# Performance work log

Measured on AMD Instinct MI355X. Metric: run time of the kernel, lower is better.

## Reference

```python
import jax, jax.numpy as jnp
import numpy as np

BATCH, HID, STEPS = 64, 2048, 30

def setup_inputs() -> dict:
    key = jax.random.key(0)
    ks = jax.random.split(key, 7)
    s = 1.0 / np.sqrt(HID)  # pytorch LSTM/Linear init scale
    return {
        "monthly_token": jax.random.normal(ks[0], (BATCH, HID), jnp.float32),
        "steps": STEPS,
        "W_ih": jax.random.uniform(ks[1], (4 * HID, HID), jnp.float32, -s, s),
        "W_hh": jax.random.uniform(ks[2], (4 * HID, HID), jnp.float32, -s, s),
        "b_ih": jax.random.uniform(ks[3], (4 * HID,), jnp.float32, -s, s),
        "b_hh": jax.random.uniform(ks[4], (4 * HID,), jnp.float32, -s, s),
        "W_out": jax.random.uniform(ks[5], (1, HID), jnp.float32, -s, s),
        "b_out": jax.random.uniform(ks[6], (1,), jnp.float32, -s, s),
    }

def reference(monthly_token, steps, W_ih, W_hh, b_ih, b_hh, W_out, b_out):
    H = monthly_token.shape[1]
    h0 = monthly_token                      # (B, H) initial hidden
    c0 = jnp.zeros_like(h0)
    x0 = jnp.zeros_like(h0)                 # first lstm input is zeros

    def step(carry, _):
        h, c, x = carry
        # PyTorch gate order: input, forget, cell(g), output
        gates = x @ W_ih.T + b_ih + h @ W_hh.T + b_hh   # (B, 4H)
        i, f, g, o = jnp.split(gates, 4, axis=-1)
        i = jax.nn.sigmoid(i)
        f = jax.nn.sigmoid(f)
        g = jnp.tanh(g)
        o = jax.nn.sigmoid(o)
        c_new = f * c + i * g
        h_new = o * jnp.tanh(c_new)
        y = h_new @ W_out.T + b_out          # (B, 1) daily value
        # feedback: next input is the lstm output (= h_new for 1-layer LSTM)
        return (h_new, c_new, h_new), y[:, 0]

    _, ys = jax.lax.scan(step, (h0, c0, x0), xs=None, length=steps)
    return ys.T                               # (B, steps)
```

## Files before the change

kernel.cpp:

```cpp
#include <hip/hip_runtime.h>
#include <cmath>


#define HID   2048
#define BATCH 64
#define G4    8192
#define NCU   256
#define HGRP  (HID * BATCH / 8)

typedef __attribute__((ext_vector_type(8))) _Float16 half8;
typedef __attribute__((ext_vector_type(4))) float f32x4;

#define LDS_BYTES 160768

__global__ void k_init(const float* __restrict__ token, const float* __restrict__ bih,
                       const float* __restrict__ bhh, half8* __restrict__ h0p,
                       float* __restrict__ bsum, unsigned* __restrict__ flags) {
    int g = blockIdx.x * 256 + threadIdx.x;
    int l = g & 63, nt = (g >> 6) & 3, kt = g >> 8;
    int n = nt * 16 + (l & 15);
    int k0 = kt * 32 + (l >> 4) * 8;
    const float4* ps = (const float4*)(token + (size_t)n * HID + k0);
    float4 a = ps[0], b = ps[1];
    half8 v;
    v[0]=(_Float16)a.x; v[1]=(_Float16)a.y; v[2]=(_Float16)a.z; v[3]=(_Float16)a.w;
    v[4]=(_Float16)b.x; v[5]=(_Float16)b.y; v[6]=(_Float16)b.z; v[7]=(_Float16)b.w;
    h0p[g] = v;
    if (g < G4) bsum[g] = bih[g] + bhh[g];
    if (g < NCU) flags[g] = 0u;
}

__global__ __launch_bounds__(512, 2)
void k_lstm(const float* __restrict__ wih, const float* __restrict__ whh,
            const float* __restrict__ bsum, const float* __restrict__ wout,
            _Float16* __restrict__ hbuf,
            float* __restrict__ ypart,
            unsigned* __restrict__ flags, int steps) {
    extern __shared__ char smem[];
    half8*     Wlds   = (half8*)smem;
    float*     gates  = (float*)(smem + 131072);
    f32x4*     red4   = (f32x4*)(smem + 139264);
    float*     cbuf   = (float*)(smem + 155648);
    float*     ybuf   = (float*)(smem + 157696);
    _Float16*  hstage = (_Float16*)(smem + 159744);

    const int tid  = threadIdx.x;
    const int blk  = blockIdx.x;
    const int lane = tid & 63;
    const int w    = tid >> 6;
    const int half = w & 1;
    const int ks   = w >> 1;

    for (int idx = tid; idx < 2 * 64 * 64; idx += 512) {
        int l = idx & 63, kt = (idx >> 6) & 63, m2 = idx >> 12;
        int m = l & 15;
        int gate = m2 * 2 + (m >> 3);
        int row  = gate * HID + blk * 8 + (m & 7);
        int col  = kt * 32 + (l >> 4) * 8;
        const float4* p = (const float4*)(whh + (size_t)row * HID + col);
        float4 a = p[0], b = p[1];
        half8 v;
        v[0]=(_Float16)a.x; v[1]=(_Float16)a.y; v[2]=(_Float16)a.z; v[3]=(_Float16)a.w;
        v[4]=(_Float16)b.x; v[5]=(_Float16)b.y; v[6]=(_Float16)b.z; v[7]=(_Float16)b.w;
        Wlds[idx] = v;
    }
    cbuf[tid] = 0.0f;

    float bias_r[2][4];
    if (ks == 0) {
        const int q = lane >> 4;
        #pragma unroll
        for (int mt2 = 0; mt2 < 2; ++mt2)
            #pragma unroll
            for (int r = 0; r < 4; ++r) {
                int m16 = q * 4 + r;
                bias_r[mt2][r] = bsum[(mt2 * 2 + (m16 >> 3)) * HID + blk * 8 + (m16 & 7)];
            }
    }
    const float wj = wout[blk * 8 + w];
    __syncthreads();

    for (int t = 0; t < steps; ++t) {
        const half8* hp = (const half8*)(hbuf + (size_t)t * HID * BATCH);
        f32x4 a00 = {0,0,0,0}, a01 = {0,0,0,0}, a10 = {0,0,0,0}, a11 = {0,0,0,0};
        const int ktb = ks * 16;
        #pragma unroll 8
        for (int kk = 0; kk < 16; ++kk) {
            int kt = ktb + kk;
            half8 av0 = Wlds[(kt) * 64 + lane];
            half8 av1 = Wlds[(64 + kt) * 64 + lane];
            half8 b0  = hp[(kt * 4 + half * 2 + 0) * 64 + lane];
            half8 b1  = hp[(kt * 4 + half * 2 + 1) * 64 + lane];
            a00 = __builtin_amdgcn_mfma_f32_16x16x32_f16(av0, b0, a00, 0, 0, 0);
            a01 = __builtin_amdgcn_mfma_f32_16x16x32_f16(av0, b1, a01, 0, 0, 0);
            a10 = __builtin_amdgcn_mfma_f32_16x16x32_f16(av1, b0, a10, 0, 0, 0);
            a11 = __builtin_amdgcn_mfma_f32_16x16x32_f16(av1, b1, a11, 0, 0, 0);
        }
        if (ks == 1 || ks == 3) {
            int srow = (ks == 3 ? 2 : 0) + half;
            red4[(srow * 4 + 0) * 64 + lane] = a00;
            red4[(srow * 4 + 1) * 64 + lane] = a01;
            red4[(srow * 4 + 2) * 64 + lane] = a10;
            red4[(srow * 4 + 3) * 64 + lane] = a11;
        }
        __syncthreads();
        if (ks == 0 || ks == 2) {
            int srow = (ks == 2 ? 2 : 0) + half;
            a00 += red4[(srow * 4 + 0) * 64 + lane];
            a01 += red4[(srow * 4 + 1) * 64 + lane];
            a10 += red4[(srow * 4 + 2) * 64 + lane];
            a11 += red4[(srow * 4 + 3) * 64 + lane];
        }
        __syncthreads();
        if (ks == 2) {
            red4[(half * 4 + 0) * 64 + lane] = a00;
            red4[(half * 4 + 1) * 64 + lane] = a01;
            red4[(half * 4 + 2) * 64 + lane] = a10;
            red4[(half * 4 + 3) * 64 + lane] = a11;
        }
        __syncthreads();
        if (ks == 0) {
            a00 += red4[(half * 4 + 0) * 64 + lane];
            a01 += red4[(half * 4 + 1) * 64 + lane];
            a10 += red4[(half * 4 + 2) * 64 + lane];
            a11 += red4[(half * 4 + 3) * 64 + lane];
            const int q = lane >> 4, col = lane & 15;
            #pragma unroll
            for (int r = 0; r < 4; ++r) {
                float* g0 = gates + (q * 4 + r) * 64 + (half * 2) * 16 + col;
                float* g1 = gates + (16 + q * 4 + r) * 64 + (half * 2) * 16 + col;
                g0[0]  = a00[r] + bias_r[0][r];
                g0[16] = a01[r] + bias_r[0][r];
                g1[0]  = a10[r] + bias_r[1][r];
                g1[16] = a11[r] + bias_r[1][r];
            }
        }
        __syncthreads();
        {
            const int b = lane;
            float gi = gates[(0  + w) * 64 + b];
            float gf = gates[(8  + w) * 64 + b];
            float gg = gates[(16 + w) * 64 + b];
            float go = gates[(24 + w) * 64 + b];
            float iv = 1.0f / (1.0f + __expf(-gi));
            float fv = 1.0f / (1.0f + __expf(-gf));
            float gv = tanhf(gg);
            float ov = 1.0f / (1.0f + __expf(-go));
            float cn = fv * cbuf[w * 64 + b] + iv * gv;
            cbuf[w * 64 + b] = cn;
            float hv = ov * tanhf(cn);
            hstage[b * 8 + w] = (_Float16)hv;
            ybuf[w * 64 + b]  = hv * wj;
        }
        __syncthreads();
        if (tid < 64) {
            float s = ybuf[tid];
            #pragma unroll
            for (int u = 1; u < 8; ++u) s += ybuf[u * 64 + tid];
            ypart[((size_t)t * NCU + blk) * 64 + tid] = s;
            const int b = tid;
            const int kt = blk >> 2, quad = blk & 3;
            const int nt = b >> 4, lp = quad * 16 + (b & 15);
            const size_t g = (size_t)(kt * 4 + nt) * 64 + lp;
            unsigned long long* dst = (unsigned long long*)
                (hbuf + (size_t)(t + 1) * HID * BATCH + g * 8);
            const unsigned long long* src =
                (const unsigned long long*)(hstage + b * 8);
            unsigned long long v0 = src[0], v1 = src[1];
            __hip_atomic_store(dst,     v0, __ATOMIC_RELAXED, __HIP_MEMORY_SCOPE_AGENT);
            __hip_atomic_store(dst + 1, v1, __ATOMIC_RELAXED, __HIP_MEMORY_SCOPE_AGENT);
        }
        if (t == 0) {
            for (int idx = tid; idx < 2 * 64 * 64; idx += 512) {
                int l = idx & 63, kt = (idx >> 6) & 63, m2 = idx >> 12;
                int m = l & 15;
                int gate = m2 * 2 + (m >> 3);
                int row  = gate * HID + blk * 8 + (m & 7);
                int col  = kt * 32 + (l >> 4) * 8;
                const float4* p = (const float4*)(wih + (size_t)row * HID + col);
                float4 a = p[0], b = p[1];
                half8 v = Wlds[idx];
                v[0] = (_Float16)((float)v[0] + a.x); v[1] = (_Float16)((float)v[1] + a.y);
                v[2] = (_Float16)((float)v[2] + a.z); v[3] = (_Float16)((float)v[3] + a.w);
                v[4] = (_Float16)((float)v[4] + b.x); v[5] = (_Float16)((float)v[5] + b.y);
                v[6] = (_Float16)((float)v[6] + b.z); v[7] = (_Float16)((float)v[7] + b.w);
                Wlds[idx] = v;
            }
        }
        if (t < steps - 1) {
            if (tid < 64) asm volatile("s_waitcnt vmcnt(0)" ::: "memory");
            if (tid == 0)
                __hip_atomic_store(&flags[blk], (unsigned)(t + 1),
                                   __ATOMIC_RELAXED, __HIP_MEMORY_SCOPE_AGENT);
            if (tid < NCU) {
                while (__hip_atomic_load(&flags[tid], __ATOMIC_RELAXED,
                                         __HIP_MEMORY_SCOPE_AGENT) <= (unsigned)t)
                    __builtin_amdgcn_s_sleep(1);
            }
            __syncthreads();
        }
    }
}

__global__ void k_yout(const float* __restrict__ ypart, const float* __restrict__ bout,
                       float* __restrict__ out, int steps) {
    int t = blockIdx.x;
    int b = threadIdx.x;
    const float* p = ypart + (size_t)t * NCU * 64 + b;
    float s = bout[0];
    #pragma unroll 8
    for (int cu = 0; cu < NCU; ++cu) s += p[(size_t)cu * 64];
    out[(size_t)b * steps + t] = s;
}

extern "C" void kernel_launch(void* const* d_in, const int* in_sizes, int n_in,
                              void* d_out, int out_size, void* d_ws, size_t ws_size,
                              hipStream_t stream) {
    const float* token = (const float*)d_in[0];
    const float* wih   = (const float*)d_in[2];
    const float* whh   = (const float*)d_in[3];
    const float* bih   = (const float*)d_in[4];
    const float* bhh   = (const float*)d_in[5];
    const float* wout  = (const float*)d_in[6];
    const float* bout  = (const float*)d_in[7];
    float* out = (float*)d_out;
    const int steps = out_size / BATCH;

    char* ws = (char*)d_ws;
    size_t off = 0;
    auto carve = [&](size_t bytes) -> void* {
        void* p = ws + off;
        off = (off + bytes + 255) & ~(size_t)255;
        return p;
    };
    _Float16* hbuf  = (_Float16*)carve((size_t)(steps + 1) * HID * BATCH * 2);
    float*    bsum  = (float*)carve((size_t)G4 * 4);
    float*    ypart = (float*)carve((size_t)steps * NCU * 64 * 4);
    unsigned* flags = (unsigned*)carve(NCU * 4);

    hipFuncSetAttribute(reinterpret_cast<const void*>(&k_lstm),
                        hipFuncAttributeMaxDynamicSharedMemorySize, LDS_BYTES);

    k_init<<<dim3(HGRP / 256), dim3(256), 0, stream>>>(
        token, bih, bhh, (half8*)hbuf, bsum, flags);

    k_lstm<<<dim3(NCU), dim3(512), LDS_BYTES, stream>>>(
        wih, whh, bsum, wout, hbuf, ypart, flags, steps);

    k_yout<<<dim3(steps), dim3(64), 0, stream>>>(ypart, bout, out, steps);
}
```

Measured before the change: 468.8 us.

## Replace grid barrier with per-wave dependency polling and parallelize output reduction

Each wave now spins only on the flags of the 64 blocks that produce the hidden-state slice it reads, so the block-wide __syncthreads after the grid barrier goes away. The flag is published right after the h stores complete, before the per-block y partial sum, which shortens the critical path between steps. The k-loop is fully unrolled, and k_yout now uses 512 threads with a shared-memory reduction instead of a serial 256-term loop. The risk is subtler memory ordering, since waves advance without a block-level barrier and the flag uses relaxed atomics.

```diff
diff --git a/kernel.cpp b/kernel.cpp
--- a/kernel.cpp
+++ b/kernel.cpp
@@ -84,7 +84,7 @@
         const half8* hp = (const half8*)(hbuf + (size_t)t * HID * BATCH);
         f32x4 a00 = {0,0,0,0}, a01 = {0,0,0,0}, a10 = {0,0,0,0}, a11 = {0,0,0,0};
         const int ktb = ks * 16;
-        #pragma unroll 8
+        #pragma unroll
         for (int kk = 0; kk < 16; ++kk) {
             int kt = ktb + kk;
             half8 av0 = Wlds[(kt) * 64 + lane];
@@ -153,12 +153,8 @@
             ybuf[w * 64 + b]  = hv * wj;
         }
         __syncthreads();
-        if (tid < 64) {
-            float s = ybuf[tid];
-            #pragma unroll
-            for (int u = 1; u < 8; ++u) s += ybuf[u * 64 + tid];
-            ypart[((size_t)t * NCU + blk) * 64 + tid] = s;
-            const int b = tid;
+        if (w == 0) {
+            const int b = lane;
             const int kt = blk >> 2, quad = blk & 3;
             const int nt = b >> 4, lp = quad * 16 + (b & 15);
             const size_t g = (size_t)(kt * 4 + nt) * 64 + lp;
@@ -169,6 +165,14 @@
             unsigned long long v0 = src[0], v1 = src[1];
             __hip_atomic_store(dst,     v0, __ATOMIC_RELAXED, __HIP_MEMORY_SCOPE_AGENT);
             __hip_atomic_store(dst + 1, v1, __ATOMIC_RELAXED, __HIP_MEMORY_SCOPE_AGENT);
+            asm volatile("s_waitcnt vmcnt(0)" ::: "memory");
+            if (lane == 0 && t < steps - 1)
+                __hip_atomic_store(&flags[blk], (unsigned)(t + 1),
+                                   __ATOMIC_RELAXED, __HIP_MEMORY_SCOPE_AGENT);
+            float s = ybuf[lane];
+            #pragma unroll
+            for (int u = 1; u < 8; ++u) s += ybuf[u * 64 + lane];
+            ypart[((size_t)t * NCU + blk) * 64 + lane] = s;
         }
         if (t == 0) {
             for (int idx = tid; idx < 2 * 64 * 64; idx += 512) {
@@ -186,31 +190,36 @@
                 v[6] = (_Float16)((float)v[6] + b.z); v[7] = (_Float16)((float)v[7] + b.w);
                 Wlds[idx] = v;
             }
+            __syncthreads();
         }
         if (t < steps - 1) {
-            if (tid < 64) asm volatile("s_waitcnt vmcnt(0)" ::: "memory");
-            if (tid == 0)
-                __hip_atomic_store(&flags[blk], (unsigned)(t + 1),
-                                   __ATOMIC_RELAXED, __HIP_MEMORY_SCOPE_AGENT);
-            if (tid < NCU) {
-                while (__hip_atomic_load(&flags[tid], __ATOMIC_RELAXED,
-                                         __HIP_MEMORY_SCOPE_AGENT) <= (unsigned)t)
-                    __builtin_amdgcn_s_sleep(1);
-            }
-            __syncthreads();
-        }
-    }
-}
-
-__global__ void k_yout(const float* __restrict__ ypart, const float* __restrict__ bout,
-                       float* __restrict__ out, int steps) {
+            while (__hip_atomic_load(&flags[ks * 64 + lane], __ATOMIC_RELAXED,
+                                     __HIP_MEMORY_SCOPE_AGENT) <= (unsigned)t)
+                __builtin_amdgcn_s_sleep(1);
+            asm volatile("" ::: "memory");
+        }
+    }
+}
+
+__global__ __launch_bounds__(512)
+void k_yout(const float* __restrict__ ypart, const float* __restrict__ bout,
+            float* __restrict__ out, int steps) {
+    __shared__ float red[8][64];
     int t = blockIdx.x;
-    int b = threadIdx.x;
+    int tid = threadIdx.x;
+    int b = tid & 63, ch = tid >> 6;
     const float* p = ypart + (size_t)t * NCU * 64 + b;
-    float s = bout[0];
+    float s = 0.0f;
     #pragma unroll 8
-    for (int cu = 0; cu < NCU; ++cu) s += p[(size_t)cu * 64];
-    out[(size_t)b * steps + t] = s;
+    for (int cu = ch * 32; cu < ch * 32 + 32; ++cu) s += p[(size_t)cu * 64];
+    red[ch][b] = s;
+    __syncthreads();
+    if (tid < 64) {
+        float r = bout[0];
+        #pragma unroll
+        for (int u = 0; u < 8; ++u) r += red[u][tid];
+        out[(size_t)tid * steps + t] = r;
+    }
 }
 
 extern "C" void kernel_launch(void* const* d_in, const int* in_sizes, int n_in,
@@ -247,5 +256,5 @@
     k_lstm<<<dim3(NCU), dim3(512), LDS_BYTES, stream>>>(
         wih, whh, bsum, wout, hbuf, ypart, flags, steps);
 
-    k_yout<<<dim3(steps), dim3(64), 0, stream>>>(ypart, bout, out, steps);
-}
+    k_yout<<<dim3(steps), dim3(512), 0, stream>>>(ypart, bout, out, steps);
+}
```

Result: faster. 450.7 us (-3.8%).
